# Kernel tuning notes

Hardware: AMD Instinct MI355X
Metric: run time of the kernel (lower is better)

## Reference

```python
import jax, jax.numpy as jnp
import numpy as np

B, T = 4, 96
IN_DIM, OUT_DIM, HID = 16, 16, 16
REL = 2 * IN_DIM  # until=True -> cat(interval max, interval min)
BIG = 1e9


def interval_pooling(a, reduction):
    # a: [b, t, t, d]; out[b,i,j] = reduce over a[b,k,l] for all i<=k<=l<=j
    t = a.shape[1]
    mask = jnp.triu(jnp.ones((t, t), dtype=bool))[None, :, :, None]
    if reduction == 'max':
        fill, cum = -BIG, jax.lax.cummax
    else:
        fill, cum = BIG, jax.lax.cummin
    x = jnp.where(mask, a, fill)
    x = cum(x, axis=1, reverse=True)  # over start k >= i
    x = cum(x, axis=2)                # over end   l <= j
    return jnp.where(mask, x, 0.0)


def dp_step(f, r, W, b):
    # linear_input[b,i,k,j] = cat(f[b,i,k], r[b,k,j]); MLPLogic = Linear+sigmoid;
    # transition_pooling_2d1d = max over k (dim 2). Split W so the wide cubic
    # concat is never materialized (same math as cat + matmul).
    df = f.shape[-1]
    Wf, Wr = W[:df], W[df:]
    ft = jnp.einsum('bikd,dh->bikh', f, Wf)[:, :, :, None, :]  # [b,i,k,1,h]
    rt = jnp.einsum('bkjd,dh->bkjh', r, Wr)[:, None, :, :, :]  # [b,1,k,j,h]
    g = jax.nn.sigmoid(ft + rt + b)  # [b, t+1, t+1, t+1, h] cubic intermediate
    return jnp.max(g, axis=2)        # pool over transition point k


def setup_inputs() -> dict:
    key = jax.random.key(0)
    ks = jax.random.split(key, 7)
    a = jax.random.normal(ks[0], (B, T, T, IN_DIM), jnp.float32)
    W0 = 0.1 * jax.random.normal(ks[1], (REL + REL, HID), jnp.float32)
    b0 = 0.1 * jax.random.normal(ks[2], (HID,), jnp.float32)
    W1 = 0.1 * jax.random.normal(ks[3], (HID + REL + REL, HID), jnp.float32)
    b1 = 0.1 * jax.random.normal(ks[4], (HID,), jnp.float32)
    W2 = 0.1 * jax.random.normal(ks[5], (HID + REL, OUT_DIM), jnp.float32)
    b2 = 0.1 * jax.random.normal(ks[6], (OUT_DIM,), jnp.float32)
    return {'a': a, 'W0': W0, 'b0': b0, 'W1': W1, 'b1': b1, 'W2': W2, 'b2': b2}


def reference(a, W0, b0, W1, b1, W2, b2):
    bsz, t = a.shape[0], a.shape[1]
    r = jnp.concatenate([interval_pooling(a, 'max'),
                         interval_pooling(a, 'min')], axis=-1)  # [b,t,t,2*in]
    f = jnp.zeros((bsz, t + 1, t + 1, r.shape[-1]), a.dtype)
    f = f.at[:, :-1, 1:].set(r)  # pad to boundary indexing [b,t+1,t+1,rel]
    r = f
    # step 0
    f = dp_step(f, r, W0, b0)
    f = jnp.concatenate([f, r], axis=-1)  # residual_input
    # step 1
    f = dp_step(f, r, W1, b1)
    f = jnp.concatenate([f, r], axis=-1)
    # final MLPLogic
    f = jax.nn.sigmoid(f @ W2 + b2)
    return f[:, :-1, 1:]
```

## Files before the change

kernel.cpp:

```cpp
#include <hip/hip_runtime.h>
#include <hip/hip_bf16.h>

#define RS   100
#define PLS  9700
#define NP   9409

#define OFF_R  0
#define OFF_A  (OFF_R  + 4*32*PLS)
#define OFF_Bm (OFF_A  + 4*16*PLS)
#define OFF_F  (OFF_Bm + 4*16*PLS)

__device__ __forceinline__ float sigm(float x) { return 1.0f / (1.0f + __expf(-x)); }

__global__ __launch_bounds__(128) void pool_kernel(const float* __restrict__ a, float* __restrict__ R) {
    __shared__ float s[96][97];
    const int tid = threadIdx.x;
    const int b  = blockIdx.x >> 5;
    const int ch = blockIdx.x & 31;
    const int d  = ch & 15;
    const bool isMin = (ch >= 16);

    for (int idx = tid; idx < 96 * 96; idx += 128) {
        int i = idx / 96, j = idx - i * 96;
        float v = a[((size_t)(b * 96 + i) * 96 + j) * 16 + d];
        if (isMin) v = -v;
        s[i][j] = (j >= i) ? v : -1e30f;
    }
    __syncthreads();
    if (tid < 96) {
        int j = tid; float run = -1e30f;
        for (int i = 95; i >= 0; --i) { run = fmaxf(run, s[i][j]); s[i][j] = run; }
    }
    __syncthreads();
    if (tid < 96) {
        int i = tid; float run = -1e30f;
        for (int j = 0; j < 96; ++j) { run = fmaxf(run, s[i][j]); s[i][j] = run; }
    }
    __syncthreads();
    float* Rp = R + (size_t)blockIdx.x * PLS;
    for (int idx = tid; idx < 97 * 97; idx += 128) {
        int x = idx / 97, y = idx - x * 97;
        float v = 0.f;
        if (x <= 95 && y >= 1 && x <= y - 1) { v = s[x][y - 1]; if (isMin) v = -v; }
        Rp[x * RS + y] = v;
    }
}

__global__ __launch_bounds__(256) void proj0_kernel(const float* __restrict__ R, const float* __restrict__ W,
                                                    float* __restrict__ A, float* __restrict__ B) {
    const int bh = blockIdx.y, b = bh >> 4, h = bh & 15;
    const int p = blockIdx.x * 256 + threadIdx.x;
    if (p >= NP) return;
    const int x = p / 97, y = p - x * 97;
    const int off = x * RS + y;
    const float* Rb = R + (size_t)b * 32 * PLS + off;
    float accA = 0.f, accB = 0.f;
#pragma unroll
    for (int d = 0; d < 32; ++d) {
        float rv = Rb[(size_t)d * PLS];
        accA += rv * W[d * 16 + h];
        accB += rv * W[(32 + d) * 16 + h];
    }
    A[(size_t)bh * PLS + off] = accA;
    B[(size_t)bh * PLS + off] = accB;
}

__global__ __launch_bounds__(256) void proj1_kernel(const float* __restrict__ R, const float* __restrict__ F1,
                                                    const float* __restrict__ W,
                                                    float* __restrict__ A, float* __restrict__ B) {
    const int bh = blockIdx.y, b = bh >> 4, h = bh & 15;
    const int p = blockIdx.x * 256 + threadIdx.x;
    if (p >= NP) return;
    const int x = p / 97, y = p - x * 97;
    const int off = x * RS + y;
    const float* Rb = R  + (size_t)b * 32 * PLS + off;
    const float* Fb = F1 + (size_t)b * 16 * PLS + off;
    float accA = 0.f, accB = 0.f;
#pragma unroll
    for (int c = 0; c < 16; ++c) accA += Fb[(size_t)c * PLS] * W[c * 16 + h];
#pragma unroll
    for (int d = 0; d < 32; ++d) {
        float rv = Rb[(size_t)d * PLS];
        accA += rv * W[(16 + d) * 16 + h];
        accB += rv * W[(48 + d) * 16 + h];
    }
    A[(size_t)bh * PLS + off] = accA;
    B[(size_t)bh * PLS + off] = accB;
}

__global__ __launch_bounds__(256) void maxplus_kernel(const float* __restrict__ A, const float* __restrict__ Bm,
                                                      const float* __restrict__ bias, float* __restrict__ F) {
    __shared__ alignas(16) float As[97][68];
    __shared__ alignas(16) float Bs[97][68];
    const int tid = threadIdx.x;
    const int bh = blockIdx.y;
    const int h  = bh & 15;
    const int i0 = (blockIdx.x & 1) * 64;
    const int j0 = (blockIdx.x >> 1) * 64;
    const float* Ab = A  + (size_t)bh * PLS;
    const float* Bb = Bm + (size_t)bh * PLS;

    for (int idx = tid; idx < 64 * 97; idx += 256) {
        int r = idx / 97, k = idx - r * 97;
        int ii = i0 + r;
        As[k][r] = (ii < 97) ? Ab[ii * RS + k] : -1e30f;
    }
    for (int idx = tid; idx < 97 * 64; idx += 256) {
        int k = idx >> 6, c = idx & 63;
        int jj = j0 + c;
        Bs[k][c] = (jj < 97) ? Bb[k * RS + jj] : -1e30f;
    }
    __syncthreads();

    const int ty = tid >> 4, tx = tid & 15;
    float acc[4][4];
#pragma unroll
    for (int r = 0; r < 4; ++r)
#pragma unroll
        for (int c = 0; c < 4; ++c) acc[r][c] = -1e30f;

#pragma unroll 4
    for (int k = 0; k < 97; ++k) {
        const float4 a4 = *reinterpret_cast<const float4*>(&As[k][ty * 4]);
        const float4 b4 = *reinterpret_cast<const float4*>(&Bs[k][tx * 4]);
        const float ar[4] = {a4.x, a4.y, a4.z, a4.w};
        const float bc[4] = {b4.x, b4.y, b4.z, b4.w};
#pragma unroll
        for (int r = 0; r < 4; ++r)
#pragma unroll
            for (int c = 0; c < 4; ++c)
                acc[r][c] = fmaxf(acc[r][c], ar[r] + bc[c]);
    }

    const float bb = bias[h];
    float* Fb = F + (size_t)bh * PLS;
#pragma unroll
    for (int r = 0; r < 4; ++r) {
        const int row = i0 + ty * 4 + r;
        if (row > 96) continue;
        const int col0 = j0 + tx * 4;
        if (col0 + 3 <= 96) {
            float4 v;
            v.x = sigm(acc[r][0] + bb);
            v.y = sigm(acc[r][1] + bb);
            v.z = sigm(acc[r][2] + bb);
            v.w = sigm(acc[r][3] + bb);
            *reinterpret_cast<float4*>(&Fb[row * RS + col0]) = v;
        } else {
            for (int c = 0; c < 4; ++c) {
                const int col = col0 + c;
                if (col <= 96) Fb[row * RS + col] = sigm(acc[r][c] + bb);
            }
        }
    }
}

__global__ __launch_bounds__(256) void final_kernel(const float* __restrict__ R, const float* __restrict__ F2,
                                                    const float* __restrict__ W, const float* __restrict__ bias,
                                                    float* __restrict__ out) {
    const int p = blockIdx.x * 256 + threadIdx.x;
    if (p >= 4 * 96 * 96) return;
    const int oj = p % 96;
    const int t1 = p / 96;
    const int i  = t1 % 96;
    const int b  = t1 / 96;
    const int off = i * RS + (oj + 1);
    const float* Fb = F2 + (size_t)b * 16 * PLS + off;
    const float* Rb = R  + (size_t)b * 32 * PLS + off;
    float acc[16];
#pragma unroll
    for (int o = 0; o < 16; ++o) acc[o] = bias[o];
#pragma unroll
    for (int c = 0; c < 16; ++c) {
        const float fv = Fb[(size_t)c * PLS];
#pragma unroll
        for (int o = 0; o < 16; ++o) acc[o] += fv * W[c * 16 + o];
    }
#pragma unroll
    for (int d = 0; d < 32; ++d) {
        const float rv = Rb[(size_t)d * PLS];
#pragma unroll
        for (int o = 0; o < 16; ++o) acc[o] += rv * W[(16 + d) * 16 + o];
    }
    float4* dst = reinterpret_cast<float4*>(out + (size_t)p * 16);
#pragma unroll
    for (int q = 0; q < 4; ++q) {
        float4 v;
        v.x = sigm(acc[q * 4 + 0]);
        v.y = sigm(acc[q * 4 + 1]);
        v.z = sigm(acc[q * 4 + 2]);
        v.w = sigm(acc[q * 4 + 3]);
        dst[q] = v;
    }
}

extern "C" void kernel_launch(void* const* d_in, const int* in_sizes, int n_in,
                              void* d_out, int out_size, void* d_ws, size_t ws_size,
                              hipStream_t stream) {
    const float* a  = (const float*)d_in[0];
    const float* W0 = (const float*)d_in[1];
    const float* b0 = (const float*)d_in[2];
    const float* W1 = (const float*)d_in[3];
    const float* b1 = (const float*)d_in[4];
    const float* W2 = (const float*)d_in[5];
    const float* b2 = (const float*)d_in[6];
    float* ws = (float*)d_ws;
    float* out = (float*)d_out;

    hipLaunchKernelGGL(pool_kernel, dim3(128), dim3(128), 0, stream, a, ws + OFF_R);
    hipLaunchKernelGGL(proj0_kernel, dim3(37, 64), dim3(256), 0, stream,
                       ws + OFF_R, W0, ws + OFF_A, ws + OFF_Bm);
    hipLaunchKernelGGL(maxplus_kernel, dim3(4, 64), dim3(256), 0, stream,
                       ws + OFF_A, ws + OFF_Bm, b0, ws + OFF_F);
    hipLaunchKernelGGL(proj1_kernel, dim3(37, 64), dim3(256), 0, stream,
                       ws + OFF_R, ws + OFF_F, W1, ws + OFF_A, ws + OFF_Bm);
    hipLaunchKernelGGL(maxplus_kernel, dim3(4, 64), dim3(256), 0, stream,
                       ws + OFF_A, ws + OFF_Bm, b1, ws + OFF_F);
    hipLaunchKernelGGL(final_kernel, dim3(144), dim3(256), 0, stream,
                       ws + OFF_R, ws + OFF_F, W2, b2, out);
}
```

Baseline: 174.2 us.

## Fuse input projections into max-plus DP kernels

The separate projection kernels that computed A and B tiles into workspace are removed. Each max-plus block now computes its own projected rows and columns directly from R (and F1) while filling shared memory. This removes two launches and a global write/read round trip, at the cost of redundant projection work across blocks and longer latency-bound tile loads. Separate F1/F2 buffers are used so step 1 can read step 0 output while writing its own.

```diff
diff --git a/kernel.cpp b/kernel.cpp
--- a/kernel.cpp
+++ b/kernel.cpp
@@ -5,10 +5,9 @@
 #define PLS  9700
 #define NP   9409
 
-#define OFF_R  0
-#define OFF_A  (OFF_R  + 4*32*PLS)
-#define OFF_Bm (OFF_A  + 4*16*PLS)
-#define OFF_F  (OFF_Bm + 4*16*PLS)
+#define OFF_R   0
+#define OFF_F1  (OFF_R  + 4*32*PLS)
+#define OFF_F2  (OFF_F1 + 4*16*PLS)
 
 __device__ __forceinline__ float sigm(float x) { return 1.0f / (1.0f + __expf(-x)); }
 
@@ -46,69 +45,41 @@
     }
 }
 
-__global__ __launch_bounds__(256) void proj0_kernel(const float* __restrict__ R, const float* __restrict__ W,
-                                                    float* __restrict__ A, float* __restrict__ B) {
-    const int bh = blockIdx.y, b = bh >> 4, h = bh & 15;
-    const int p = blockIdx.x * 256 + threadIdx.x;
-    if (p >= NP) return;
-    const int x = p / 97, y = p - x * 97;
-    const int off = x * RS + y;
-    const float* Rb = R + (size_t)b * 32 * PLS + off;
-    float accA = 0.f, accB = 0.f;
-#pragma unroll
-    for (int d = 0; d < 32; ++d) {
-        float rv = Rb[(size_t)d * PLS];
-        accA += rv * W[d * 16 + h];
-        accB += rv * W[(32 + d) * 16 + h];
-    }
-    A[(size_t)bh * PLS + off] = accA;
-    B[(size_t)bh * PLS + off] = accB;
-}
-
-__global__ __launch_bounds__(256) void proj1_kernel(const float* __restrict__ R, const float* __restrict__ F1,
-                                                    const float* __restrict__ W,
-                                                    float* __restrict__ A, float* __restrict__ B) {
-    const int bh = blockIdx.y, b = bh >> 4, h = bh & 15;
-    const int p = blockIdx.x * 256 + threadIdx.x;
-    if (p >= NP) return;
-    const int x = p / 97, y = p - x * 97;
-    const int off = x * RS + y;
-    const float* Rb = R  + (size_t)b * 32 * PLS + off;
-    const float* Fb = F1 + (size_t)b * 16 * PLS + off;
-    float accA = 0.f, accB = 0.f;
-#pragma unroll
-    for (int c = 0; c < 16; ++c) accA += Fb[(size_t)c * PLS] * W[c * 16 + h];
-#pragma unroll
-    for (int d = 0; d < 32; ++d) {
-        float rv = Rb[(size_t)d * PLS];
-        accA += rv * W[(16 + d) * 16 + h];
-        accB += rv * W[(48 + d) * 16 + h];
-    }
-    A[(size_t)bh * PLS + off] = accA;
-    B[(size_t)bh * PLS + off] = accB;
-}
-
-__global__ __launch_bounds__(256) void maxplus_kernel(const float* __restrict__ A, const float* __restrict__ Bm,
-                                                      const float* __restrict__ bias, float* __restrict__ F) {
+__global__ __launch_bounds__(256) void maxplus0_kernel(const float* __restrict__ R, const float* __restrict__ W,
+                                                       const float* __restrict__ bias, float* __restrict__ F) {
     __shared__ alignas(16) float As[97][68];
     __shared__ alignas(16) float Bs[97][68];
     const int tid = threadIdx.x;
-    const int bh = blockIdx.y;
-    const int h  = bh & 15;
+    const int bh = blockIdx.y, b = bh >> 4, h = bh & 15;
     const int i0 = (blockIdx.x & 1) * 64;
     const int j0 = (blockIdx.x >> 1) * 64;
-    const float* Ab = A  + (size_t)bh * PLS;
-    const float* Bb = Bm + (size_t)bh * PLS;
+    const float* Rb = R + (size_t)b * 32 * PLS;
 
     for (int idx = tid; idx < 64 * 97; idx += 256) {
         int r = idx / 97, k = idx - r * 97;
         int ii = i0 + r;
-        As[k][r] = (ii < 97) ? Ab[ii * RS + k] : -1e30f;
+        float v = -1e30f;
+        if (ii < 97) {
+            const int off = ii * RS + k;
+            float acc = 0.f;
+#pragma unroll
+            for (int d = 0; d < 32; ++d) acc += Rb[(size_t)d * PLS + off] * W[d * 16 + h];
+            v = acc;
+        }
+        As[k][r] = v;
     }
     for (int idx = tid; idx < 97 * 64; idx += 256) {
         int k = idx >> 6, c = idx & 63;
         int jj = j0 + c;
-        Bs[k][c] = (jj < 97) ? Bb[k * RS + jj] : -1e30f;
+        float v = -1e30f;
+        if (jj < 97) {
+            const int off = k * RS + jj;
+            float acc = 0.f;
+#pragma unroll
+            for (int d = 0; d < 32; ++d) acc += Rb[(size_t)d * PLS + off] * W[(32 + d) * 16 + h];
+            v = acc;
+        }
+        Bs[k][c] = v;
     }
     __syncthreads();
 
@@ -155,6 +126,91 @@
     }
 }
 
+__global__ __launch_bounds__(256) void maxplus1_kernel(const float* __restrict__ R, const float* __restrict__ F1,
+                                                       const float* __restrict__ W, const float* __restrict__ bias,
+                                                       float* __restrict__ F) {
+    __shared__ alignas(16) float As[97][68];
+    __shared__ alignas(16) float Bs[97][68];
+    const int tid = threadIdx.x;
+    const int bh = blockIdx.y, b = bh >> 4, h = bh & 15;
+    const int i0 = (blockIdx.x & 1) * 64;
+    const int j0 = (blockIdx.x >> 1) * 64;
+    const float* Rb = R  + (size_t)b * 32 * PLS;
+    const float* Fb1 = F1 + (size_t)b * 16 * PLS;
+
+    for (int idx = tid; idx < 64 * 97; idx += 256) {
+        int r = idx / 97, k = idx - r * 97;
+        int ii = i0 + r;
+        float v = -1e30f;
+        if (ii < 97) {
+            const int off = ii * RS + k;
+            float acc = 0.f;
+#pragma unroll
+            for (int c = 0; c < 16; ++c) acc += Fb1[(size_t)c * PLS + off] * W[c * 16 + h];
+#pragma unroll
+            for (int d = 0; d < 32; ++d) acc += Rb[(size_t)d * PLS + off] * W[(16 + d) * 16 + h];
+            v = acc;
+        }
+        As[k][r] = v;
+    }
+    for (int idx = tid; idx < 97 * 64; idx += 256) {
+        int k = idx >> 6, c = idx & 63;
+        int jj = j0 + c;
+        float v = -1e30f;
+        if (jj < 97) {
+            const int off = k * RS + jj;
+            float acc = 0.f;
+#pragma unroll
+            for (int d = 0; d < 32; ++d) acc += Rb[(size_t)d * PLS + off] * W[(48 + d) * 16 + h];
+            v = acc;
+        }
+        Bs[k][c] = v;
+    }
+    __syncthreads();
+
+    const int ty = tid >> 4, tx = tid & 15;
+    float acc[4][4];
+#pragma unroll
+    for (int r = 0; r < 4; ++r)
+#pragma unroll
+        for (int c = 0; c < 4; ++c) acc[r][c] = -1e30f;
+
+#pragma unroll 4
+    for (int k = 0; k < 97; ++k) {
+        const float4 a4 = *reinterpret_cast<const float4*>(&As[k][ty * 4]);
+        const float4 b4 = *reinterpret_cast<const float4*>(&Bs[k][tx * 4]);
+        const float ar[4] = {a4.x, a4.y, a4.z, a4.w};
+        const float bc[4] = {b4.x, b4.y, b4.z, b4.w};
+#pragma unroll
+        for (int r = 0; r < 4; ++r)
+#pragma unroll
+            for (int c = 0; c < 4; ++c)
+                acc[r][c] = fmaxf(acc[r][c], ar[r] + bc[c]);
+    }
+
+    const float bb = bias[h];
+    float* Fb = F + (size_t)bh * PLS;
+#pragma unroll
+    for (int r = 0; r < 4; ++r) {
+        const int row = i0 + ty * 4 + r;
+        if (row > 96) continue;
+        const int col0 = j0 + tx * 4;
+        if (col0 + 3 <= 96) {
+            float4 v;
+            v.x = sigm(acc[r][0] + bb);
+            v.y = sigm(acc[r][1] + bb);
+            v.z = sigm(acc[r][2] + bb);
+            v.w = sigm(acc[r][3] + bb);
+            *reinterpret_cast<float4*>(&Fb[row * RS + col0]) = v;
+        } else {
+            for (int c = 0; c < 4; ++c) {
+                const int col = col0 + c;
+                if (col <= 96) Fb[row * RS + col] = sigm(acc[r][c] + bb);
+            }
+        }
+    }
+}
+
 __global__ __launch_bounds__(256) void final_kernel(const float* __restrict__ R, const float* __restrict__ F2,
                                                     const float* __restrict__ W, const float* __restrict__ bias,
                                                     float* __restrict__ out) {
@@ -208,14 +264,10 @@
     float* out = (float*)d_out;
 
     hipLaunchKernelGGL(pool_kernel, dim3(128), dim3(128), 0, stream, a, ws + OFF_R);
-    hipLaunchKernelGGL(proj0_kernel, dim3(37, 64), dim3(256), 0, stream,
-                       ws + OFF_R, W0, ws + OFF_A, ws + OFF_Bm);
-    hipLaunchKernelGGL(maxplus_kernel, dim3(4, 64), dim3(256), 0, stream,
-                       ws + OFF_A, ws + OFF_Bm, b0, ws + OFF_F);
-    hipLaunchKernelGGL(proj1_kernel, dim3(37, 64), dim3(256), 0, stream,
-                       ws + OFF_R, ws + OFF_F, W1, ws + OFF_A, ws + OFF_Bm);
-    hipLaunchKernelGGL(maxplus_kernel, dim3(4, 64), dim3(256), 0, stream,
-                       ws + OFF_A, ws + OFF_Bm, b1, ws + OFF_F);
+    hipLaunchKernelGGL(maxplus0_kernel, dim3(4, 64), dim3(256), 0, stream,
+                       ws + OFF_R, W0, b0, ws + OFF_F1);
+    hipLaunchKernelGGL(maxplus1_kernel, dim3(4, 64), dim3(256), 0, stream,
+                       ws + OFF_R, ws + OFF_F1, W1, b1, ws + OFF_F2);
     hipLaunchKernelGGL(final_kernel, dim3(144), dim3(256), 0, stream,
-                       ws + OFF_R, ws + OFF_F, W2, b2, out);
-}
+                       ws + OFF_R, ws + OFF_F2, W2, b2, out);
+}
```

New measurement: 207.0 us. 1.19x slower.
